# Performance work log

Measured on AMD Instinct MI355X. Metric: run time of the kernel, lower is better.

The kernel has to match this reference:

```python
import jax, jax.numpy as jnp
import numpy as np

B, S, F = 4, 4096, 128
GAMMA = 0.96875


def setup_inputs() -> dict:
    key = jax.random.key(0)
    ks = jax.random.split(key, 8)
    x = jax.random.normal(ks[0], (B, S, F), dtype=jnp.float32)
    # torch nn.Linear params: W [out,in], b [out]
    lim = 1.0 / np.sqrt(F)
    Wq = jax.random.uniform(ks[1], (F, F), jnp.float32, -lim, lim)
    bq = jax.random.uniform(ks[2], (F,), jnp.float32, -lim, lim)
    Wk = jax.random.uniform(ks[3], (F, F), jnp.float32, -lim, lim)
    bk = jax.random.uniform(ks[4], (F,), jnp.float32, -lim, lim)
    Wv = jax.random.uniform(ks[5], (F, F), jnp.float32, -lim, lim)
    bv = jax.random.uniform(ks[6], (F,), jnp.float32, -lim, lim)
    theta = jax.random.uniform(ks[7], (1, F), jnp.float32)  # th.rand
    return {"x": x, "Wq": Wq, "bq": bq, "Wk": Wk, "bk": bk, "Wv": Wv, "bv": bv, "theta": theta}


def _masks(Sn, theta, dtype):
    # rotary-like phase: index [S,1] @ theta [1,F] -> [S,F]
    idx = jnp.arange(1, Sn + 1, dtype=dtype)[:, None]
    mt = idx * theta  # broadcasted outer product, [S,F]
    cos, sin = jnp.cos(mt), jnp.sin(mt)
    # causal exponential decay mask: gamma**(i-j) for i>=j else 0
    i = jnp.arange(Sn)[:, None]
    j = jnp.arange(Sn)[None, :]
    e = i - j
    decay = jnp.where(e >= 0, jnp.asarray(GAMMA, dtype) ** jnp.maximum(e, 0).astype(dtype), jnp.asarray(0.0, dtype))
    return cos, sin, decay


def reference(x, Wq, bq, Wk, bk, Wv, bv, theta):
    Bn, Sn, Fn = x.shape
    q = x @ Wq.T + bq
    k = x @ Wk.T + bk
    v = x @ Wv.T + bv
    cos, sin, decay = _masks(Sn, theta, x.dtype)
    # retention scores: QK^T under cos/sin modulation, [B,S,S]
    scores = jnp.einsum('bsf,btf->bst', q * cos, k * cos) \
           + jnp.einsum('bsf,btf->bst', q * sin, k * sin)
    scores = scores * decay
    return jnp.einsum('bst,btf->bsf', scores, v)
```

## Files before the change

kernel.cpp:

```cpp
#include <hip/hip_runtime.h>


#define S_LEN 4096
#define B_N   4
#define F_N   128
#define WIN   384
#define LOG2_GAMMA (-0.0458036905705339f)

typedef unsigned short u16;
typedef unsigned int   u32;
typedef __attribute__((ext_vector_type(8))) short bf16x8;
typedef __attribute__((ext_vector_type(4))) float f32x4;

__device__ inline u16 f2bf(float x) {
    u32 u = __builtin_bit_cast(u32, x);
    u32 r = (u + 0x7fffu + ((u >> 16) & 1u)) >> 16;
    return (u16)r;
}
__device__ inline u32 pkbf(float a, float b) {
    return (u32)f2bf(a) | ((u32)f2bf(b) << 16);
}

__global__ void prep_kernel(const float* __restrict__ Wq,
                            const float* __restrict__ Wk,
                            const float* __restrict__ Wv,
                            u16* __restrict__ WbF)
{
    const int idx    = blockIdx.x * 256 + threadIdx.x;
    const int lane   = idx & 63;
    const int fragid = idx >> 6;
    const int ks     = fragid & 3;
    const int nt     = (fragid >> 2) & 7;
    const int mat    = fragid >> 5;
    const float* W = (mat == 0) ? Wq : (mat == 1 ? Wk : Wv);
    const float* src = W + (nt * 16 + (lane & 15)) * F_N + ks * 32 + (lane >> 4) * 8;
    float4 a = *(const float4*)src;
    float4 b = *(const float4*)(src + 4);
    uint4 v = make_uint4(pkbf(a.x, a.y), pkbf(a.z, a.w),
                         pkbf(b.x, b.y), pkbf(b.z, b.w));
    *(uint4*)(WbF + fragid * 512 + lane * 8) = v;
}

__global__ __launch_bounds__(256)
void proj_kernel(const float* __restrict__ x, const u16* __restrict__ WbF,
                 const float* __restrict__ bq, const float* __restrict__ bk,
                 const float* __restrict__ bv, const float* __restrict__ theta,
                 u16* __restrict__ QbF, u16* __restrict__ KbF,
                 u16* __restrict__ VtF)
{
    __shared__ __align__(16) u16 obQ[32 * 264];
    __shared__ __align__(16) u16 obK[32 * 264];

    const int tid  = threadIdx.x;
    const int lane = tid & 63;
    const int w    = __builtin_amdgcn_readfirstlane(tid >> 6);
    const int r0   = blockIdx.x * 32;
    const int b    = r0 >> 12;
    const int s0   = r0 & (S_LEN - 1);
    const int col  = lane & 15;
    const int quad = lane >> 4;
    const int mt   = w & 1;
    const int nh   = w >> 1;

    bf16x8 af[4];
    const float* xr = x + (r0 + mt * 16 + col) * F_N + quad * 8;
#pragma unroll
    for (int ks = 0; ks < 4; ++ks) {
        float4 a = *(const float4*)(xr + ks * 32);
        float4 c = *(const float4*)(xr + ks * 32 + 4);
        uint4 u = make_uint4(pkbf(a.x, a.y), pkbf(a.z, a.w),
                             pkbf(c.x, c.y), pkbf(c.z, c.w));
        af[ks] = __builtin_bit_cast(bf16x8, u);
    }

    f32x4 qa[4], ka[4], va[4];
#pragma unroll
    for (int nt = 0; nt < 4; ++nt) {
        qa[nt] = (f32x4){0.f, 0.f, 0.f, 0.f};
        ka[nt] = (f32x4){0.f, 0.f, 0.f, 0.f};
        va[nt] = (f32x4){0.f, 0.f, 0.f, 0.f};
    }
#pragma unroll
    for (int nt = 0; nt < 4; ++nt) {
        const int ng = nh * 4 + nt;
#pragma unroll
        for (int ks = 0; ks < 4; ++ks) {
            bf16x8 bqf = *(const bf16x8*)(WbF + ((0 * 8 + ng) * 4 + ks) * 512 + lane * 8);
            bf16x8 bkf = *(const bf16x8*)(WbF + ((1 * 8 + ng) * 4 + ks) * 512 + lane * 8);
            bf16x8 bvf = *(const bf16x8*)(WbF + ((2 * 8 + ng) * 4 + ks) * 512 + lane * 8);
            qa[nt] = __builtin_amdgcn_mfma_f32_16x16x32_bf16(af[ks], bqf, qa[nt], 0, 0, 0);
            ka[nt] = __builtin_amdgcn_mfma_f32_16x16x32_bf16(af[ks], bkf, ka[nt], 0, 0, 0);
            va[nt] = __builtin_amdgcn_mfma_f32_16x16x32_bf16(af[ks], bvf, va[nt], 0, 0, 0);
        }
    }

#pragma unroll
    for (int nt = 0; nt < 4; ++nt) {
        const int o = nh * 64 + nt * 16 + col;
        const float bqv = bq[o], bkv = bk[o], th = theta[o];
#pragma unroll
        for (int r = 0; r < 4; ++r) {
            const int srow = s0 + mt * 16 + quad * 4 + r;
            float sn, cs;
            __sincosf((float)(srow + 1) * th, &sn, &cs);
            const float q = qa[nt][r] + bqv;
            const float k = ka[nt][r] + bkv;
            const int row = mt * 16 + quad * 4 + r;
            obQ[row * 264 + o]       = f2bf(q * cs);
            obQ[row * 264 + 128 + o] = f2bf(q * sn);
            obK[row * 264 + o]       = f2bf(k * cs);
            obK[row * 264 + 128 + o] = f2bf(k * sn);
        }
    }
    __syncthreads();
#pragma unroll
    for (int it = 0; it < 4; ++it) {
        const int c  = it * 256 + tid;
        const int gl = c >> 9;
        const int ks = (c >> 6) & 7;
        const int ln = c & 63;
        const int a  = (gl * 16 + (ln & 15)) * 264 + ks * 32 + (ln >> 4) * 8;
        const long dst = (long)((b * 256 + (s0 >> 4) + gl) * 8 + ks) * 512 + ln * 8;
        *(uint4*)(QbF + dst) = *(const uint4*)(obQ + a);
        *(uint4*)(KbF + dst) = *(const uint4*)(obK + a);
    }
    __syncthreads();

#pragma unroll
    for (int nt = 0; nt < 4; ++nt) {
        const int f = nh * 64 + nt * 16 + col;
        const float bvv = bv[f];
#pragma unroll
        for (int r = 0; r < 4; ++r) {
            const int sl = mt * 16 + quad * 4 + r;
            obQ[f * 40 + sl] = f2bf(va[nt][r] + bvv);
        }
    }
    __syncthreads();
#pragma unroll
    for (int it = 0; it < 2; ++it) {
        const int c  = it * 256 + tid;
        const int ft = c >> 6;
        const int ln = c & 63;
        uint4 v = *(const uint4*)(obQ + (ft * 16 + (ln & 15)) * 40 + (ln >> 4) * 8);
        *(uint4*)(VtF + ((long)((b * 128 + (s0 >> 5)) * 8 + ft)) * 512 + ln * 8) = v;
    }
}

__global__ __launch_bounds__(256)
void retention_kernel(const u16* __restrict__ QbF, const u16* __restrict__ KbF,
                      const u16* __restrict__ VtF, float* __restrict__ out)
{
    __shared__ __align__(16) u16 P_lds[32 * 72];

    const int tid  = threadIdx.x;
    const int lane = tid & 63;
    const int w    = __builtin_amdgcn_readfirstlane(tid >> 6);
    const int b    = blockIdx.y;
    const int s0   = blockIdx.x * 32;
    const int col  = lane & 15;
    const int quad = lane >> 4;
    const int ssub = (w & 1) * 16;
    const int fh   = w >> 1;

    const int t_start = (s0 >= WIN) ? ((s0 - WIN) & ~63) : 0;
    const int nch     = (s0 + 32 - t_start + 63) >> 6;

    const int g = (s0 + ssub) >> 4;
    bf16x8 qf[8];
#pragma unroll
    for (int ks = 0; ks < 8; ++ks)
        qf[ks] = *(const bf16x8*)(QbF + ((long)((b * 256 + g) * 8 + ks)) * 512 + lane * 8);

    f32x4 oacc[4];
#pragma unroll
    for (int ft = 0; ft < 4; ++ft) oacc[ft] = (f32x4){0.f, 0.f, 0.f, 0.f};

    for (int ch = 0; ch < nch; ++ch) {
        const int tc = t_start + (ch << 6);

        f32x4 pacc[2];
#pragma unroll
        for (int tp = 0; tp < 2; ++tp) {
            const int tg = (tc >> 4) + fh * 2 + tp;
            const u16* kb = KbF + ((long)(b * 256 + tg) * 8) * 512 + lane * 8;
            f32x4 acc = (f32x4){0.f, 0.f, 0.f, 0.f};
#pragma unroll
            for (int ks = 0; ks < 8; ++ks) {
                bf16x8 kf = *(const bf16x8*)(kb + ks * 512);
                acc = __builtin_amdgcn_mfma_f32_16x16x32_bf16(qf[ks], kf, acc, 0, 0, 0);
            }
            pacc[tp] = acc;
        }
        __syncthreads();

#pragma unroll
        for (int tp = 0; tp < 2; ++tp) {
            const int tglob = tc + (fh * 2 + tp) * 16 + col;
#pragma unroll
            for (int r = 0; r < 4; ++r) {
                const int e = (s0 + ssub + quad * 4 + r) - tglob;
                const float d = (e >= 0) ? exp2f((float)e * LOG2_GAMMA) : 0.f;
                P_lds[(ssub + quad * 4 + r) * 72 + (fh * 2 + tp) * 16 + col] =
                    f2bf(pacc[tp][r] * d);
            }
        }
        __syncthreads();

#pragma unroll
        for (int ks = 0; ks < 2; ++ks) {
            bf16x8 pa = *(const bf16x8*)(P_lds + (ssub + col) * 72 + ks * 32 + quad * 8);
            const int tb = (tc >> 5) + ks;
#pragma unroll
            for (int ft = 0; ft < 4; ++ft) {
                bf16x8 vb = *(const bf16x8*)(VtF +
                    ((long)((b * 128 + tb) * 8 + fh * 4 + ft)) * 512 + lane * 8);
                oacc[ft] = __builtin_amdgcn_mfma_f32_16x16x32_bf16(pa, vb, oacc[ft], 0, 0, 0);
            }
        }
    }

    float* ob = out + ((b << 12) + s0) * F_N;
#pragma unroll
    for (int ft = 0; ft < 4; ++ft)
#pragma unroll
        for (int r = 0; r < 4; ++r)
            ob[(ssub + quad * 4 + r) * F_N + fh * 64 + ft * 16 + col] = oacc[ft][r];
}

extern "C" void kernel_launch(void* const* d_in, const int* in_sizes, int n_in,
                              void* d_out, int out_size, void* d_ws, size_t ws_size,
                              hipStream_t stream) {
    const float* x     = (const float*)d_in[0];
    const float* Wq    = (const float*)d_in[1];
    const float* bq    = (const float*)d_in[2];
    const float* Wk    = (const float*)d_in[3];
    const float* bk    = (const float*)d_in[4];
    const float* Wv    = (const float*)d_in[5];
    const float* bv    = (const float*)d_in[6];
    const float* theta = (const float*)d_in[7];
    float* out = (float*)d_out;

    u16* ws  = (u16*)d_ws;
    u16* QbF = ws;
    u16* KbF = ws + 4194304;
    u16* VtF = ws + 8388608;
    u16* WbF = ws + 10485760;

    prep_kernel<<<24, 256, 0, stream>>>(Wq, Wk, Wv, WbF);
    proj_kernel<<<512, 256, 0, stream>>>(x, WbF, bq, bk, bv, theta, QbF, KbF, VtF);
    retention_kernel<<<dim3(128, B_N), 256, 0, stream>>>(QbF, KbF, VtF, out);
}
```

Baseline: 116.8 us.

## Fuse projection and retention into one kernel with per-chunk K/V recompute in LDS

Replaces the three-kernel pipeline (weight prep, QKV projection to global, retention) with a single kernel. Each block projects its own 64-row Q tile, then for each 128-row key chunk in the decay window recomputes the K and V projections directly from x and fp32 weights into LDS. It then does the score and PV MFMAs from LDS. This removes global round-trips of bf16 Q/K/V and two launches, at the cost of redundant K/V projection work, repeated fp32 weight loads and conversions, and only one 512-thread block per CU.

```diff
diff --git a/kernel.cpp b/kernel.cpp
--- a/kernel.cpp
+++ b/kernel.cpp
@@ -20,212 +20,185 @@
 __device__ inline u32 pkbf(float a, float b) {
     return (u32)f2bf(a) | ((u32)f2bf(b) << 16);
 }
-
-__global__ void prep_kernel(const float* __restrict__ Wq,
-                            const float* __restrict__ Wk,
-                            const float* __restrict__ Wv,
-                            u16* __restrict__ WbF)
+__device__ inline bf16x8 frag8(const float* p) {
+    float4 a = *(const float4*)p;
+    float4 b = *(const float4*)(p + 4);
+    uint4 u = make_uint4(pkbf(a.x, a.y), pkbf(a.z, a.w),
+                         pkbf(b.x, b.y), pkbf(b.z, b.w));
+    return __builtin_bit_cast(bf16x8, u);
+}
+
+#define SK 266
+#define SV 130
+
+__global__ __launch_bounds__(512)
+void retention_fused(const float* __restrict__ x,
+                     const float* __restrict__ Wq, const float* __restrict__ bq,
+                     const float* __restrict__ Wk, const float* __restrict__ bk,
+                     const float* __restrict__ Wv, const float* __restrict__ bv,
+                     const float* __restrict__ theta,
+                     float* __restrict__ out)
 {
-    const int idx    = blockIdx.x * 256 + threadIdx.x;
-    const int lane   = idx & 63;
-    const int fragid = idx >> 6;
-    const int ks     = fragid & 3;
-    const int nt     = (fragid >> 2) & 7;
-    const int mat    = fragid >> 5;
-    const float* W = (mat == 0) ? Wq : (mat == 1 ? Wk : Wv);
-    const float* src = W + (nt * 16 + (lane & 15)) * F_N + ks * 32 + (lane >> 4) * 8;
-    float4 a = *(const float4*)src;
-    float4 b = *(const float4*)(src + 4);
-    uint4 v = make_uint4(pkbf(a.x, a.y), pkbf(a.z, a.w),
-                         pkbf(b.x, b.y), pkbf(b.z, b.w));
-    *(uint4*)(WbF + fragid * 512 + lane * 8) = v;
-}
-
-__global__ __launch_bounds__(256)
-void proj_kernel(const float* __restrict__ x, const u16* __restrict__ WbF,
-                 const float* __restrict__ bq, const float* __restrict__ bk,
-                 const float* __restrict__ bv, const float* __restrict__ theta,
-                 u16* __restrict__ QbF, u16* __restrict__ KbF,
-                 u16* __restrict__ VtF)
-{
-    __shared__ __align__(16) u16 obQ[32 * 264];
-    __shared__ __align__(16) u16 obK[32 * 264];
+    __shared__ __align__(16) u16 Kp[128 * SK];
+    __shared__ __align__(16) u16 Vt[128 * SV];
+    __shared__ __align__(16) u16 Pl[64 * SV];
 
     const int tid  = threadIdx.x;
     const int lane = tid & 63;
     const int w    = __builtin_amdgcn_readfirstlane(tid >> 6);
-    const int r0   = blockIdx.x * 32;
-    const int b    = r0 >> 12;
-    const int s0   = r0 & (S_LEN - 1);
     const int col  = lane & 15;
     const int quad = lane >> 4;
-    const int mt   = w & 1;
-    const int nh   = w >> 1;
-
-    bf16x8 af[4];
-    const float* xr = x + (r0 + mt * 16 + col) * F_N + quad * 8;
-#pragma unroll
-    for (int ks = 0; ks < 4; ++ks) {
-        float4 a = *(const float4*)(xr + ks * 32);
-        float4 c = *(const float4*)(xr + ks * 32 + 4);
-        uint4 u = make_uint4(pkbf(a.x, a.y), pkbf(a.z, a.w),
-                             pkbf(c.x, c.y), pkbf(c.z, c.w));
-        af[ks] = __builtin_bit_cast(bf16x8, u);
-    }
-
-    f32x4 qa[4], ka[4], va[4];
+    const int bid  = blockIdx.x;
+    const int b    = bid >> 6;
+    const int r6   = bid & 63;
+    const int s_tile = (r6 & 7) * 8 + (r6 >> 3);
+    const int s0   = s_tile * 64;
+    const int mt4  = w & 3;
+    const int half = w >> 2;
+    const int ssub = mt4 * 16;
+
+    const float* xb = x + (long)b * (S_LEN * F_N);
+
+    bf16x8 xfq[4];
+    {
+        const float* xr = xb + (s0 + ssub + col) * F_N + quad * 8;
+#pragma unroll
+        for (int ks = 0; ks < 4; ++ks) xfq[ks] = frag8(xr + ks * 32);
+    }
+    f32x4 qacc[4];
+#pragma unroll
+    for (int nt = 0; nt < 4; ++nt) qacc[nt] = (f32x4){0.f, 0.f, 0.f, 0.f};
 #pragma unroll
     for (int nt = 0; nt < 4; ++nt) {
-        qa[nt] = (f32x4){0.f, 0.f, 0.f, 0.f};
-        ka[nt] = (f32x4){0.f, 0.f, 0.f, 0.f};
-        va[nt] = (f32x4){0.f, 0.f, 0.f, 0.f};
+        const float* wp = Wq + ((half * 4 + nt) * 16 + col) * F_N + quad * 8;
+#pragma unroll
+        for (int ks = 0; ks < 4; ++ks) {
+            bf16x8 wf = frag8(wp + ks * 32);
+            qacc[nt] = __builtin_amdgcn_mfma_f32_16x16x32_bf16(xfq[ks], wf, qacc[nt], 0, 0, 0);
+        }
     }
 #pragma unroll
     for (int nt = 0; nt < 4; ++nt) {
-        const int ng = nh * 4 + nt;
-#pragma unroll
-        for (int ks = 0; ks < 4; ++ks) {
-            bf16x8 bqf = *(const bf16x8*)(WbF + ((0 * 8 + ng) * 4 + ks) * 512 + lane * 8);
-            bf16x8 bkf = *(const bf16x8*)(WbF + ((1 * 8 + ng) * 4 + ks) * 512 + lane * 8);
-            bf16x8 bvf = *(const bf16x8*)(WbF + ((2 * 8 + ng) * 4 + ks) * 512 + lane * 8);
-            qa[nt] = __builtin_amdgcn_mfma_f32_16x16x32_bf16(af[ks], bqf, qa[nt], 0, 0, 0);
-            ka[nt] = __builtin_amdgcn_mfma_f32_16x16x32_bf16(af[ks], bkf, ka[nt], 0, 0, 0);
-            va[nt] = __builtin_amdgcn_mfma_f32_16x16x32_bf16(af[ks], bvf, va[nt], 0, 0, 0);
-        }
-    }
-
-#pragma unroll
-    for (int nt = 0; nt < 4; ++nt) {
-        const int o = nh * 64 + nt * 16 + col;
-        const float bqv = bq[o], bkv = bk[o], th = theta[o];
+        const int o = half * 64 + nt * 16 + col;
+        const float bqv = bq[o], th = theta[o];
 #pragma unroll
         for (int r = 0; r < 4; ++r) {
-            const int srow = s0 + mt * 16 + quad * 4 + r;
+            const int row = ssub + quad * 4 + r;
             float sn, cs;
-            __sincosf((float)(srow + 1) * th, &sn, &cs);
-            const float q = qa[nt][r] + bqv;
-            const float k = ka[nt][r] + bkv;
-            const int row = mt * 16 + quad * 4 + r;
-            obQ[row * 264 + o]       = f2bf(q * cs);
-            obQ[row * 264 + 128 + o] = f2bf(q * sn);
-            obK[row * 264 + o]       = f2bf(k * cs);
-            obK[row * 264 + 128 + o] = f2bf(k * sn);
+            __sincosf((float)(s0 + row + 1) * th, &sn, &cs);
+            const float q = qacc[nt][r] + bqv;
+            Kp[row * SK + o]       = f2bf(q * cs);
+            Kp[row * SK + 128 + o] = f2bf(q * sn);
         }
     }
     __syncthreads();
-#pragma unroll
-    for (int it = 0; it < 4; ++it) {
-        const int c  = it * 256 + tid;
-        const int gl = c >> 9;
-        const int ks = (c >> 6) & 7;
-        const int ln = c & 63;
-        const int a  = (gl * 16 + (ln & 15)) * 264 + ks * 32 + (ln >> 4) * 8;
-        const long dst = (long)((b * 256 + (s0 >> 4) + gl) * 8 + ks) * 512 + ln * 8;
-        *(uint4*)(QbF + dst) = *(const uint4*)(obQ + a);
-        *(uint4*)(KbF + dst) = *(const uint4*)(obK + a);
-    }
+    bf16x8 qf[8];
+#pragma unroll
+    for (int ks = 0; ks < 8; ++ks)
+        qf[ks] = *(const bf16x8*)(Kp + (ssub + col) * SK + ks * 32 + quad * 8);
     __syncthreads();
 
-#pragma unroll
-    for (int nt = 0; nt < 4; ++nt) {
-        const int f = nh * 64 + nt * 16 + col;
-        const float bvv = bv[f];
-#pragma unroll
-        for (int r = 0; r < 4; ++r) {
-            const int sl = mt * 16 + quad * 4 + r;
-            obQ[f * 40 + sl] = f2bf(va[nt][r] + bvv);
-        }
-    }
-    __syncthreads();
-#pragma unroll
-    for (int it = 0; it < 2; ++it) {
-        const int c  = it * 256 + tid;
-        const int ft = c >> 6;
-        const int ln = c & 63;
-        uint4 v = *(const uint4*)(obQ + (ft * 16 + (ln & 15)) * 40 + (ln >> 4) * 8);
-        *(uint4*)(VtF + ((long)((b * 128 + (s0 >> 5)) * 8 + ft)) * 512 + ln * 8) = v;
-    }
-}
-
-__global__ __launch_bounds__(256)
-void retention_kernel(const u16* __restrict__ QbF, const u16* __restrict__ KbF,
-                      const u16* __restrict__ VtF, float* __restrict__ out)
-{
-    __shared__ __align__(16) u16 P_lds[32 * 72];
-
-    const int tid  = threadIdx.x;
-    const int lane = tid & 63;
-    const int w    = __builtin_amdgcn_readfirstlane(tid >> 6);
-    const int b    = blockIdx.y;
-    const int s0   = blockIdx.x * 32;
-    const int col  = lane & 15;
-    const int quad = lane >> 4;
-    const int ssub = (w & 1) * 16;
-    const int fh   = w >> 1;
-
-    const int t_start = (s0 >= WIN) ? ((s0 - WIN) & ~63) : 0;
-    const int nch     = (s0 + 32 - t_start + 63) >> 6;
-
-    const int g = (s0 + ssub) >> 4;
-    bf16x8 qf[8];
-#pragma unroll
-    for (int ks = 0; ks < 8; ++ks)
-        qf[ks] = *(const bf16x8*)(QbF + ((long)((b * 256 + g) * 8 + ks)) * 512 + lane * 8);
+    const int t_start = (s0 >= WIN) ? ((s0 - WIN) & ~127) : 0;
+    const int nch     = (s0 + 64 - t_start + 127) >> 7;
 
     f32x4 oacc[4];
 #pragma unroll
     for (int ft = 0; ft < 4; ++ft) oacc[ft] = (f32x4){0.f, 0.f, 0.f, 0.f};
 
     for (int ch = 0; ch < nch; ++ch) {
-        const int tc = t_start + (ch << 6);
-
-        f32x4 pacc[2];
-#pragma unroll
-        for (int tp = 0; tp < 2; ++tp) {
-            const int tg = (tc >> 4) + fh * 2 + tp;
-            const u16* kb = KbF + ((long)(b * 256 + tg) * 8) * 512 + lane * 8;
-            f32x4 acc = (f32x4){0.f, 0.f, 0.f, 0.f};
+        const int tc = t_start + (ch << 7);
+
+        bf16x8 xf[2][4];
+#pragma unroll
+        for (int m = 0; m < 2; ++m) {
+            const int tl = (mt4 + m * 4) * 16;
+            const float* xr = xb + (tc + tl + col) * F_N + quad * 8;
+#pragma unroll
+            for (int ks = 0; ks < 4; ++ks) xf[m][ks] = frag8(xr + ks * 32);
+        }
+        f32x4 kacc[2][4], vacc[2][4];
+#pragma unroll
+        for (int m = 0; m < 2; ++m)
+#pragma unroll
+            for (int nt = 0; nt < 4; ++nt) {
+                kacc[m][nt] = (f32x4){0.f, 0.f, 0.f, 0.f};
+                vacc[m][nt] = (f32x4){0.f, 0.f, 0.f, 0.f};
+            }
+#pragma unroll
+        for (int nt = 0; nt < 4; ++nt) {
+            const float* wkp = Wk + ((half * 4 + nt) * 16 + col) * F_N + quad * 8;
+            const float* wvp = Wv + ((half * 4 + nt) * 16 + col) * F_N + quad * 8;
+#pragma unroll
+            for (int ks = 0; ks < 4; ++ks) {
+                bf16x8 wkf = frag8(wkp + ks * 32);
+                bf16x8 wvf = frag8(wvp + ks * 32);
+#pragma unroll
+                for (int m = 0; m < 2; ++m) {
+                    kacc[m][nt] = __builtin_amdgcn_mfma_f32_16x16x32_bf16(xf[m][ks], wkf, kacc[m][nt], 0, 0, 0);
+                    vacc[m][nt] = __builtin_amdgcn_mfma_f32_16x16x32_bf16(xf[m][ks], wvf, vacc[m][nt], 0, 0, 0);
+                }
+            }
+        }
+#pragma unroll
+        for (int m = 0; m < 2; ++m)
+#pragma unroll
+            for (int nt = 0; nt < 4; ++nt) {
+                const int o = half * 64 + nt * 16 + col;
+                const float bkv = bk[o], bvv = bv[o], th = theta[o];
+#pragma unroll
+                for (int r = 0; r < 4; ++r) {
+                    const int tl = (mt4 + m * 4) * 16 + quad * 4 + r;
+                    float sn, cs;
+                    __sincosf((float)(tc + tl + 1) * th, &sn, &cs);
+                    const float k = kacc[m][nt][r] + bkv;
+                    Kp[tl * SK + o]       = f2bf(k * cs);
+                    Kp[tl * SK + 128 + o] = f2bf(k * sn);
+                    Vt[o * SV + tl]       = f2bf(vacc[m][nt][r] + bvv);
+                }
+            }
+        __syncthreads();
+
+#pragma unroll
+        for (int tt = 0; tt < 4; ++tt) {
+            const int tb = half * 64 + tt * 16;
+            f32x4 pacc = (f32x4){0.f, 0.f, 0.f, 0.f};
 #pragma unroll
             for (int ks = 0; ks < 8; ++ks) {
-                bf16x8 kf = *(const bf16x8*)(kb + ks * 512);
-                acc = __builtin_amdgcn_mfma_f32_16x16x32_bf16(qf[ks], kf, acc, 0, 0, 0);
-            }
-            pacc[tp] = acc;
-        }
-        __syncthreads();
-
-#pragma unroll
-        for (int tp = 0; tp < 2; ++tp) {
-            const int tglob = tc + (fh * 2 + tp) * 16 + col;
+                bf16x8 kf = *(const bf16x8*)(Kp + (tb + col) * SK + ks * 32 + quad * 8);
+                pacc = __builtin_amdgcn_mfma_f32_16x16x32_bf16(qf[ks], kf, pacc, 0, 0, 0);
+            }
+            const int tglob = tc + tb + col;
 #pragma unroll
             for (int r = 0; r < 4; ++r) {
                 const int e = (s0 + ssub + quad * 4 + r) - tglob;
                 const float d = (e >= 0) ? exp2f((float)e * LOG2_GAMMA) : 0.f;
-                P_lds[(ssub + quad * 4 + r) * 72 + (fh * 2 + tp) * 16 + col] =
-                    f2bf(pacc[tp][r] * d);
+                Pl[(ssub + quad * 4 + r) * SV + tb + col] = f2bf(pacc[r] * d);
             }
         }
         __syncthreads();
 
-#pragma unroll
-        for (int ks = 0; ks < 2; ++ks) {
-            bf16x8 pa = *(const bf16x8*)(P_lds + (ssub + col) * 72 + ks * 32 + quad * 8);
-            const int tb = (tc >> 5) + ks;
-#pragma unroll
-            for (int ft = 0; ft < 4; ++ft) {
-                bf16x8 vb = *(const bf16x8*)(VtF +
-                    ((long)((b * 128 + tb) * 8 + fh * 4 + ft)) * 512 + lane * 8);
-                oacc[ft] = __builtin_amdgcn_mfma_f32_16x16x32_bf16(pa, vb, oacc[ft], 0, 0, 0);
-            }
-        }
-    }
-
-    float* ob = out + ((b << 12) + s0) * F_N;
+        bf16x8 pa[4];
+#pragma unroll
+        for (int ks = 0; ks < 4; ++ks)
+            pa[ks] = *(const bf16x8*)(Pl + (ssub + col) * SV + ks * 32 + quad * 8);
+#pragma unroll
+        for (int ft = 0; ft < 4; ++ft) {
+#pragma unroll
+            for (int ks = 0; ks < 4; ++ks) {
+                bf16x8 vb = *(const bf16x8*)(Vt + (half * 64 + ft * 16 + col) * SV +
+                                             ks * 32 + quad * 8);
+                oacc[ft] = __builtin_amdgcn_mfma_f32_16x16x32_bf16(pa[ks], vb, oacc[ft], 0, 0, 0);
+            }
+        }
+        __syncthreads();
+    }
+
+    float* ob = out + ((long)(b << 12) + s0) * F_N;
 #pragma unroll
     for (int ft = 0; ft < 4; ++ft)
 #pragma unroll
         for (int r = 0; r < 4; ++r)
-            ob[(ssub + quad * 4 + r) * F_N + fh * 64 + ft * 16 + col] = oacc[ft][r];
+            ob[(ssub + quad * 4 + r) * F_N + half * 64 + ft * 16 + col] = oacc[ft][r];
 }
 
 extern "C" void kernel_launch(void* const* d_in, const int* in_sizes, int n_in,
@@ -241,13 +214,6 @@
     const float* theta = (const float*)d_in[7];
     float* out = (float*)d_out;
 
-    u16* ws  = (u16*)d_ws;
-    u16* QbF = ws;
-    u16* KbF = ws + 4194304;
-    u16* VtF = ws + 8388608;
-    u16* WbF = ws + 10485760;
-
-    prep_kernel<<<24, 256, 0, stream>>>(Wq, Wk, Wv, WbF);
-    proj_kernel<<<512, 256, 0, stream>>>(x, WbF, bq, bk, bv, theta, QbF, KbF, VtF);
-    retention_kernel<<<dim3(128, B_N), 256, 0, stream>>>(QbF, KbF, VtF, out);
-}
+    retention_fused<<<B_N * 64, 512, 0, stream>>>(x, Wq, bq, Wk, bk, Wv, bv,
+                                                  theta, out);
+}
```

Result: slower. 156.1 us (+33.7%).

## Split retention key chunks across waves with LDS reduction, 16-row blocks

Applied to the files above, without the earlier changes.

The retention kernel now gives each block 16 query rows instead of 32, doubling the grid. Each wave handles a disjoint subset of 32-key chunks, so the per-chunk __syncthreads barriers are gone. Partial outputs are reduced through shared memory at the end. The decay factor is now a precomputed per-lane table times one exp2 per chunk, instead of an exp2 per element. In exchange there is extra LDS traffic for the reduction, K/V tiles are re-read by twice as many blocks, and the load across waves is uneven for short windows.

```diff
diff --git a/kernel.cpp b/kernel.cpp
--- a/kernel.cpp
+++ b/kernel.cpp
@@ -147,85 +147,108 @@
     }
 }
 
-__global__ __launch_bounds__(256)
+__global__ __launch_bounds__(256, 4)
 void retention_kernel(const u16* __restrict__ QbF, const u16* __restrict__ KbF,
                       const u16* __restrict__ VtF, float* __restrict__ out)
 {
-    __shared__ __align__(16) u16 P_lds[32 * 72];
+    __shared__ __align__(16) u16   Pl[4 * 16 * 40];
+    __shared__ __align__(16) float Ored[3 * 2048];
 
     const int tid  = threadIdx.x;
     const int lane = tid & 63;
     const int w    = __builtin_amdgcn_readfirstlane(tid >> 6);
     const int b    = blockIdx.y;
-    const int s0   = blockIdx.x * 32;
+    const int s0   = blockIdx.x * 16;
     const int col  = lane & 15;
     const int quad = lane >> 4;
-    const int ssub = (w & 1) * 16;
-    const int fh   = w >> 1;
-
-    const int t_start = (s0 >= WIN) ? ((s0 - WIN) & ~63) : 0;
-    const int nch     = (s0 + 32 - t_start + 63) >> 6;
-
-    const int g = (s0 + ssub) >> 4;
+
     bf16x8 qf[8];
 #pragma unroll
     for (int ks = 0; ks < 8; ++ks)
-        qf[ks] = *(const bf16x8*)(QbF + ((long)((b * 256 + g) * 8 + ks)) * 512 + lane * 8);
-
-    f32x4 oacc[4];
-#pragma unroll
-    for (int ft = 0; ft < 4; ++ft) oacc[ft] = (f32x4){0.f, 0.f, 0.f, 0.f};
-
-    for (int ch = 0; ch < nch; ++ch) {
-        const int tc = t_start + (ch << 6);
+        qf[ks] = *(const bf16x8*)(QbF + ((long)((b * 256 + (s0 >> 4)) * 8 + ks)) * 512 + lane * 8);
+
+    float Adec[2][4];
+    int   eoff[2][4];
+#pragma unroll
+    for (int tt = 0; tt < 2; ++tt)
+#pragma unroll
+        for (int r = 0; r < 4; ++r) {
+            eoff[tt][r] = quad * 4 + r - tt * 16 - col;
+            Adec[tt][r] = exp2f((float)eoff[tt][r] * LOG2_GAMMA);
+        }
+
+    int t_start = 0;
+    if (s0 >= WIN) t_start = (s0 - WIN) & ~31;
+    const int n32 = (s0 + 16 - t_start + 31) >> 5;
+
+    f32x4 oacc[8];
+#pragma unroll
+    for (int ft = 0; ft < 8; ++ft) oacc[ft] = (f32x4){0.f, 0.f, 0.f, 0.f};
+
+    u16* myP = Pl + w * (16 * 40);
+
+    for (int i = w; i < n32; i += 4) {
+        const int tc = t_start + i * 32;
+        const int eb = s0 - tc;
+        const float pb = exp2f((float)eb * LOG2_GAMMA);
 
         f32x4 pacc[2];
 #pragma unroll
-        for (int tp = 0; tp < 2; ++tp) {
-            const int tg = (tc >> 4) + fh * 2 + tp;
-            const u16* kb = KbF + ((long)(b * 256 + tg) * 8) * 512 + lane * 8;
+        for (int tt = 0; tt < 2; ++tt) {
+            const u16* kb = KbF + ((long)((b * 256 + (tc >> 4) + tt)) * 8) * 512 + lane * 8;
             f32x4 acc = (f32x4){0.f, 0.f, 0.f, 0.f};
 #pragma unroll
             for (int ks = 0; ks < 8; ++ks) {
                 bf16x8 kf = *(const bf16x8*)(kb + ks * 512);
                 acc = __builtin_amdgcn_mfma_f32_16x16x32_bf16(qf[ks], kf, acc, 0, 0, 0);
             }
-            pacc[tp] = acc;
-        }
-        __syncthreads();
-
-#pragma unroll
-        for (int tp = 0; tp < 2; ++tp) {
-            const int tglob = tc + (fh * 2 + tp) * 16 + col;
+            pacc[tt] = acc;
+        }
+
+#pragma unroll
+        for (int tt = 0; tt < 2; ++tt)
 #pragma unroll
             for (int r = 0; r < 4; ++r) {
-                const int e = (s0 + ssub + quad * 4 + r) - tglob;
-                const float d = (e >= 0) ? exp2f((float)e * LOG2_GAMMA) : 0.f;
-                P_lds[(ssub + quad * 4 + r) * 72 + (fh * 2 + tp) * 16 + col] =
-                    f2bf(pacc[tp][r] * d);
+                const int e = eb + eoff[tt][r];
+                const float d = (e >= 0) ? pb * Adec[tt][r] : 0.f;
+                myP[(quad * 4 + r) * 40 + tt * 16 + col] = f2bf(pacc[tt][r] * d);
             }
-        }
-        __syncthreads();
-
-#pragma unroll
-        for (int ks = 0; ks < 2; ++ks) {
-            bf16x8 pa = *(const bf16x8*)(P_lds + (ssub + col) * 72 + ks * 32 + quad * 8);
-            const int tb = (tc >> 5) + ks;
-#pragma unroll
-            for (int ft = 0; ft < 4; ++ft) {
-                bf16x8 vb = *(const bf16x8*)(VtF +
-                    ((long)((b * 128 + tb) * 8 + fh * 4 + ft)) * 512 + lane * 8);
-                oacc[ft] = __builtin_amdgcn_mfma_f32_16x16x32_bf16(pa, vb, oacc[ft], 0, 0, 0);
+
+        bf16x8 pa = *(const bf16x8*)(myP + col * 40 + quad * 8);
+        const int tb = tc >> 5;
+#pragma unroll
+        for (int ft = 0; ft < 8; ++ft) {
+            bf16x8 vb = *(const bf16x8*)(VtF +
+                ((long)((b * 128 + tb) * 8 + ft)) * 512 + lane * 8);
+            oacc[ft] = __builtin_amdgcn_mfma_f32_16x16x32_bf16(pa, vb, oacc[ft], 0, 0, 0);
+        }
+    }
+
+    if (w > 0) {
+        float* rg = Ored + (w - 1) * 2048 + lane * 4;
+#pragma unroll
+        for (int ft = 0; ft < 8; ++ft)
+            *(f32x4*)(rg + ft * 256) = oacc[ft];
+    }
+    __syncthreads();
+    if (w == 0) {
+#pragma unroll
+        for (int k = 0; k < 3; ++k) {
+            const float* rg = Ored + k * 2048 + lane * 4;
+#pragma unroll
+            for (int ft = 0; ft < 8; ++ft) {
+                f32x4 v = *(const f32x4*)(rg + ft * 256);
+                oacc[ft][0] += v[0]; oacc[ft][1] += v[1];
+                oacc[ft][2] += v[2]; oacc[ft][3] += v[3];
             }
         }
-    }
-
-    float* ob = out + ((b << 12) + s0) * F_N;
-#pragma unroll
-    for (int ft = 0; ft < 4; ++ft)
-#pragma unroll
-        for (int r = 0; r < 4; ++r)
-            ob[(ssub + quad * 4 + r) * F_N + fh * 64 + ft * 16 + col] = oacc[ft][r];
+        float* ob = out + ((long)(b << 12) + s0) * F_N;
+#pragma unroll
+        for (int ft = 0; ft < 8; ++ft)
+#pragma unroll
+            for (int r = 0; r < 4; ++r)
+                ob[(quad * 4 + r) * F_N + ft * 16 + col] = oacc[ft][r];
+    }
 }
 
 extern "C" void kernel_launch(void* const* d_in, const int* in_sizes, int n_in,
@@ -249,5 +272,5 @@
 
     prep_kernel<<<24, 256, 0, stream>>>(Wq, Wk, Wv, WbF);
     proj_kernel<<<512, 256, 0, stream>>>(x, WbF, bq, bk, bv, theta, QbF, KbF, VtF);
-    retention_kernel<<<dim3(128, B_N), 256, 0, stream>>>(QbF, KbF, VtF, out);
-}
+    retention_kernel<<<dim3(256, B_N), 256, 0, stream>>>(QbF, KbF, VtF, out);
+}
```

New measurement: 136.7 us. 17.1% more time.
